# Performance work log

Measured on AMD Instinct MI355X. Metric: run time of the kernel, lower is better.

## Reference

```python
import jax, jax.numpy as jnp
import numpy as np

EPS = 1e-5

def layer_norm(x, gamma, beta):
    mu = jnp.mean(x, axis=-1, keepdims=True)
    var = jnp.mean(jnp.square(x - mu), axis=-1, keepdims=True)
    return (x - mu) * jax.lax.rsqrt(var + EPS) * gamma + beta

def setup_inputs() -> dict:
    key = jax.random.key(0)
    ks = jax.random.split(key, 16)
    B, Cq, Hq, Wq = 8, 256, 32, 32
    Cc, Hc, Wc = 512, 64, 64
    def lin(k, fan_in, fan_out):
        lim = 1.0 / np.sqrt(fan_in)
        k1, k2 = jax.random.split(k)
        W = jax.random.uniform(k1, (fan_in, fan_out), jnp.float32, -lim, lim)
        b = jax.random.uniform(k2, (fan_out,), jnp.float32, -lim, lim)
        return W, b
    Wq_, bq = lin(ks[0], Cq, Cq)
    Wk_, bk = lin(ks[1], Cc, Cq)
    Wv_, bv = lin(ks[2], Cc, Cq)
    Wo_, bo = lin(ks[3], Cq, Cq)
    return {
        "query": jax.random.normal(ks[4], (B, Cq, Hq, Wq), jnp.float32),
        "context": jax.random.normal(ks[5], (B, Cc, Hc, Wc), jnp.float32),
        "Wq": Wq_, "bq": bq, "Wk": Wk_, "bk": bk, "Wv": Wv_, "bv": bv,
        "Wo": Wo_, "bo": bo,
        "gq": jnp.ones((Cq,), jnp.float32), "betq": jnp.zeros((Cq,), jnp.float32),
        "gc": jnp.ones((Cc,), jnp.float32), "betc": jnp.zeros((Cc,), jnp.float32),
    }

def reference(query, context, Wq, bq, Wk, bk, Wv, bv, Wo, bo, gq, betq, gc, betc):
    B, Cq, Hq, Wq_sp = query.shape
    _, Cc, Hc, Wc = context.shape
    num_heads = 8
    head_dim = Cq // num_heads
    scale = jnp.sqrt(jnp.float32(head_dim))
    N = Hq * Wq_sp
    # adaptive_avg_pool2d with divisible sizes == average pooling over equal bins
    ctx = context.reshape(B, Cc, Hq, Hc // Hq, Wq_sp, Wc // Wq_sp).mean(axis=(3, 5))
    q_flat = query.reshape(B, Cq, N).transpose(0, 2, 1)          # (B,N,Cq)
    c_flat = ctx.reshape(B, Cc, N).transpose(0, 2, 1)            # (B,N,Cc)
    qn = layer_norm(q_flat, gq, betq)
    cn = layer_norm(c_flat, gc, betc)
    q = (qn @ Wq + bq).reshape(B, N, num_heads, head_dim).transpose(0, 2, 1, 3)
    k = (cn @ Wk + bk).reshape(B, N, num_heads, head_dim).transpose(0, 2, 1, 3)
    v = (cn @ Wv + bv).reshape(B, N, num_heads, head_dim).transpose(0, 2, 1, 3)
    attn = jnp.einsum('bhnd,bhmd->bhnm', q, k) / scale
    attn = jax.nn.softmax(attn, axis=-1)
    out = jnp.einsum('bhnm,bhmd->bhnd', attn, v)
    out = out.transpose(0, 2, 1, 3).reshape(B, N, Cq)
    out = out @ Wo + bo
    out = q_flat + out                                           # residual
    return out.transpose(0, 2, 1).reshape(B, Cq, Hq, Wq_sp)
```

## Files before the change

### kernel.cpp

```cpp
#include <hip/hip_runtime.h>
#include <hip/hip_bf16.h>
#include <cstddef>

#define B_  8
#define CQ  256
#define CC  512
#define N_  1024
#define HQ  32
#define WQ  32
#define NH  8
#define HD  32

typedef __bf16 bf16x8 __attribute__((ext_vector_type(8)));
typedef float f32x4 __attribute__((ext_vector_type(4)));
typedef float f32x16 __attribute__((ext_vector_type(16)));
typedef unsigned int uint4v __attribute__((ext_vector_type(4)));
typedef unsigned short ushort8 __attribute__((ext_vector_type(8)));
typedef unsigned short ushort4v __attribute__((ext_vector_type(4)));
typedef unsigned short ushort2v __attribute__((ext_vector_type(2)));

__device__ __forceinline__ unsigned short f2bf(float x) {
    return __builtin_bit_cast(unsigned short, __float2bfloat16(x));
}
__device__ __forceinline__ float bf2f(unsigned short x) {
    return __bfloat162float(__builtin_bit_cast(__hip_bfloat16, x));
}
__device__ __forceinline__ bf16x8 ldb8(const unsigned short* p) {
    return __builtin_bit_cast(bf16x8, *(const ushort8*)p);
}

__global__ __launch_bounds__(256) void prep_k(
    const float* __restrict__ query, const float* __restrict__ context,
    const float* __restrict__ Wq, const float* __restrict__ Wk,
    const float* __restrict__ Wv, const float* __restrict__ Wo,
    const float* __restrict__ gq, const float* __restrict__ betq,
    const float* __restrict__ gc, const float* __restrict__ betc,
    __hip_bfloat16* __restrict__ Wqt, __hip_bfloat16* __restrict__ Wkt,
    __hip_bfloat16* __restrict__ Wvt, __hip_bfloat16* __restrict__ Wot,
    __hip_bfloat16* __restrict__ qn, __hip_bfloat16* __restrict__ cn) {
    __shared__ __align__(16) char sm[36352];
    const int bid = blockIdx.x;
    const int tid = threadIdx.x;

    if (bid < 512) {
        float (*T)[33] = (float (*)[33])sm;
        const int x = bid & 15, y = (bid >> 4) & 7, z = bid >> 7;
        const float* W; __hip_bfloat16* Wt; int K;
        switch (z) {
            case 0: W = Wq; Wt = Wqt; K = CQ; break;
            case 1: W = Wk; Wt = Wkt; K = CC; break;
            case 2: W = Wv; Wt = Wvt; K = CC; break;
            default: W = Wo; Wt = Wot; K = CQ; break;
        }
        const int k0 = x * 32;
        if (k0 >= K) return;
        const int c0 = y * 32;
        const int tx = tid & 31, ty = tid >> 5;
        #pragma unroll
        for (int i = 0; i < 4; ++i) {
            const int r = ty + 8 * i;
            T[r][tx] = W[(size_t)(k0 + r) * CQ + c0 + tx];
        }
        __syncthreads();
        #pragma unroll
        for (int i = 0; i < 4; ++i) {
            const int r = ty + 8 * i;
            Wt[(size_t)(c0 + r) * K + k0 + tx] = __float2bfloat16(T[tx][r]);
        }
    } else if (bid < 768) {
        const int u = bid - 512;
        const int hq = u & 31, b = u >> 5;
        unsigned short (*P)[32] = (unsigned short (*)[32])sm;
        float (*Ss)[32]  = (float (*)[32])(sm + 32768);
        float (*S2s)[32] = (float (*)[32])(sm + 33792);
        float* Mu = (float*)(sm + 34816);
        float* Rs = (float*)(sm + 34944);
        const int wq = tid & 31, cty = tid >> 5;

        const float* Cb = context + (size_t)b * CC * 64 * 64;
        float s = 0.f, s2 = 0.f;
        #pragma unroll 4
        for (int it = 0; it < 64; ++it) {
            const int cc = it * 8 + cty;
            const float* r0 = Cb + ((size_t)cc * 64 + 2 * hq) * 64 + 2 * wq;
            const float2 a  = *(const float2*)(r0);
            const float2 bv = *(const float2*)(r0 + 64);
            const float v = (a.x + a.y + bv.x + bv.y) * 0.25f;
            P[cc][wq ^ (cc & 31)] = f2bf(v);
            s += v; s2 += v * v;
        }
        Ss[cty][wq] = s; S2s[cty][wq] = s2;
        __syncthreads();
        if (cty == 0) {
            float ts = 0.f, t2 = 0.f;
            #pragma unroll
            for (int i = 0; i < 8; ++i) { ts += Ss[i][wq]; t2 += S2s[i][wq]; }
            const float mu  = ts * (1.f / CC);
            const float var = t2 * (1.f / CC) - mu * mu;
            Mu[wq] = mu; Rs[wq] = rsqrtf(var + 1e-5f);
        }
        __syncthreads();
        unsigned short* outb = (unsigned short*)cn + ((size_t)b * N_ + hq * 32) * CC;
        #pragma unroll 4
        for (int it = 0; it < 32; ++it) {
            const int idx = it * 256 + tid;
            const int row = idx >> 8;
            const int c   = (idx & 255) * 2;
            const float v0 = bf2f(P[c][row ^ (c & 31)]);
            const float v1 = bf2f(P[c + 1][row ^ ((c + 1) & 31)]);
            const float mu = Mu[row], rs = Rs[row];
            ushort2v o;
            o.x = f2bf((v0 - mu) * rs * gc[c] + betc[c]);
            o.y = f2bf((v1 - mu) * rs * gc[c + 1] + betc[c + 1]);
            *(ushort2v*)(outb + (size_t)row * CC + c) = o;
        }
    } else {
        const int u = bid - 768;
        const int n0 = (u & 15) * 64, b = u >> 4;
        unsigned short (*Qt)[264] = (unsigned short (*)[264])sm;
        float (*Ss)[64]  = (float (*)[64])(sm + 33792);
        float (*S2s)[64] = (float (*)[64])(sm + 34816);
        float* Mu = (float*)(sm + 35840);
        float* Rs = (float*)(sm + 36096);
        const int tx = tid & 63, ty = tid >> 6;

        const float* Qb = query + (size_t)b * CQ * N_;
        float s = 0.f, s2 = 0.f;
        for (int c = ty; c < CQ; c += 4) {
            const float v = Qb[(size_t)c * N_ + n0 + tx];
            Qt[tx][c] = f2bf(v);
            s += v; s2 += v * v;
        }
        Ss[ty][tx] = s; S2s[ty][tx] = s2;
        __syncthreads();
        if (ty == 0) {
            float ts = 0.f, t2 = 0.f;
            #pragma unroll
            for (int i = 0; i < 4; ++i) { ts += Ss[i][tx]; t2 += S2s[i][tx]; }
            const float mu  = ts * (1.f / CQ);
            const float var = t2 * (1.f / CQ) - mu * mu;
            Mu[tx] = mu; Rs[tx] = rsqrtf(var + 1e-5f);
        }
        __syncthreads();
        unsigned short* outb = (unsigned short*)qn + ((size_t)b * N_ + n0) * CQ;
        #pragma unroll
        for (int it = 0; it < 8; ++it) {
            const int idx = it * 256 + tid;
            const int row = idx >> 5;
            const int c0  = (idx & 31) * 8;
            const ushort8 v = *(const ushort8*)&Qt[row][c0];
            const float mu = Mu[row], rs = Rs[row];
            ushort8 o;
            #pragma unroll
            for (int e = 0; e < 8; ++e)
                o[e] = f2bf((bf2f(v[e]) - mu) * rs * gq[c0 + e] + betq[c0 + e]);
            *(ushort8*)(outb + (size_t)row * CQ + c0) = o;
        }
    }
}

__global__ __launch_bounds__(256) void proj_all_k(
    const __hip_bfloat16* __restrict__ qn, const __hip_bfloat16* __restrict__ cn,
    const __hip_bfloat16* __restrict__ Wqt, const __hip_bfloat16* __restrict__ Wkt,
    const __hip_bfloat16* __restrict__ Wvt,
    const float* __restrict__ bq, const float* __restrict__ bk,
    const float* __restrict__ bv,
    __hip_bfloat16* __restrict__ Qb, __hip_bfloat16* __restrict__ Kb,
    __hip_bfloat16* __restrict__ Vt, float qsc) {
    __shared__ unsigned short As[64][40];
    __shared__ unsigned short B1[64][40];
    __shared__ unsigned short B2[64][40];

    const int zz = blockIdx.z;
    const int n0 = blockIdx.x * 64;
    const int c0 = blockIdx.y * 64;
    const int tid = threadIdx.x;
    const int wid = tid >> 6, lane = tid & 63;
    const int lg = lane >> 4, ln = lane & 15;
    const int wn0 = (wid & 1) * 32, wc0 = (wid >> 1) * 32;
    const int sr = tid >> 2;
    const int sk = (tid & 3) * 8;

    if (zz >= 8) {
        const int b = zz - 8;
        const unsigned short* Ab = (const unsigned short*)qn + ((size_t)b * N_ + n0) * CQ;
        const unsigned short* Wb = (const unsigned short*)Wqt + (size_t)c0 * CQ;
        f32x4 acc[2][2] = {};
        ushort8 ra = *(const ushort8*)(Ab + (size_t)sr * CQ + sk);
        ushort8 rw = *(const ushort8*)(Wb + (size_t)sr * CQ + sk);
        for (int t = 0; t < 8; ++t) {
            *(ushort8*)&As[sr][sk] = ra;
            *(ushort8*)&B1[sr][sk] = rw;
            __syncthreads();
            if (t < 7) {
                ra = *(const ushort8*)(Ab + (size_t)sr * CQ + (t + 1) * 32 + sk);
                rw = *(const ushort8*)(Wb + (size_t)sr * CQ + (t + 1) * 32 + sk);
            }
            bf16x8 a[2], w[2];
            #pragma unroll
            for (int i = 0; i < 2; ++i) a[i] = ldb8(&As[wn0 + 16 * i + ln][8 * lg]);
            #pragma unroll
            for (int j = 0; j < 2; ++j) w[j] = ldb8(&B1[wc0 + 16 * j + ln][8 * lg]);
            #pragma unroll
            for (int i = 0; i < 2; ++i)
                #pragma unroll
                for (int j = 0; j < 2; ++j)
                    acc[i][j] = __builtin_amdgcn_mfma_f32_16x16x32_bf16(a[i], w[j], acc[i][j], 0, 0, 0);
            __syncthreads();
        }
        #pragma unroll
        for (int j = 0; j < 2; ++j) {
            const int co = c0 + wc0 + 16 * j + ln;
            const int h = co >> 5, d = co & 31;
            const float bb = bq[co];
            #pragma unroll
            for (int i = 0; i < 2; ++i)
                #pragma unroll
                for (int r = 0; r < 4; ++r) {
                    const int n = n0 + wn0 + 16 * i + 4 * lg + r;
                    Qb[(((size_t)b * NH + h) * N_ + n) * HD + d] =
                        __float2bfloat16((acc[i][j][r] + bb) * qsc);
                }
        }
    } else {
        const int b = zz;
        const unsigned short* Ab  = (const unsigned short*)cn + ((size_t)b * N_ + n0) * CC;
        const unsigned short* Wkb = (const unsigned short*)Wkt + (size_t)c0 * CC;
        const unsigned short* Wvb = (const unsigned short*)Wvt + (size_t)c0 * CC;
        f32x4 accK[2][2] = {};
        f32x4 accV[2][2] = {};
        ushort8 ra = *(const ushort8*)(Ab  + (size_t)sr * CC + sk);
        ushort8 rk = *(const ushort8*)(Wkb + (size_t)sr * CC + sk);
        ushort8 rv = *(const ushort8*)(Wvb + (size_t)sr * CC + sk);
        for (int t = 0; t < 16; ++t) {
            *(ushort8*)&As[sr][sk] = ra;
            *(ushort8*)&B1[sr][sk] = rk;
            *(ushort8*)&B2[sr][sk] = rv;
            __syncthreads();
            if (t < 15) {
                ra = *(const ushort8*)(Ab  + (size_t)sr * CC + (t + 1) * 32 + sk);
                rk = *(const ushort8*)(Wkb + (size_t)sr * CC + (t + 1) * 32 + sk);
                rv = *(const ushort8*)(Wvb + (size_t)sr * CC + (t + 1) * 32 + sk);
            }
            bf16x8 a[2], wk[2], wv[2];
            #pragma unroll
            for (int i = 0; i < 2; ++i) {
                a[i]  = ldb8(&As[wn0 + 16 * i + ln][8 * lg]);
                wk[i] = ldb8(&B1[wc0 + 16 * i + ln][8 * lg]);
                wv[i] = ldb8(&B2[wc0 + 16 * i + ln][8 * lg]);
            }
            #pragma unroll
            for (int i = 0; i < 2; ++i)
                #pragma unroll
                for (int j = 0; j < 2; ++j) {
                    accK[i][j] = __builtin_amdgcn_mfma_f32_16x16x32_bf16(a[i], wk[j], accK[i][j], 0, 0, 0);
                    accV[i][j] = __builtin_amdgcn_mfma_f32_16x16x32_bf16(a[i], wv[j], accV[i][j], 0, 0, 0);
                }
            __syncthreads();
        }
        #pragma unroll
        for (int j = 0; j < 2; ++j) {
            const int co = c0 + wc0 + 16 * j + ln;
            const int h = co >> 5, d = co & 31;
            const float bbk = bk[co], bbv = bv[co];
            #pragma unroll
            for (int i = 0; i < 2; ++i) {
                const int nb = n0 + wn0 + 16 * i + 4 * lg;
                #pragma unroll
                for (int r = 0; r < 4; ++r)
                    Kb[(((size_t)b * NH + h) * N_ + nb + r) * HD + d] =
                        __float2bfloat16(accK[i][j][r] + bbk);
                ushort4v o;
                #pragma unroll
                for (int r = 0; r < 4; ++r) o[r] = f2bf(accV[i][j][r] + bbv);
                const int g  = (nb >> 2) & 3;
                const int gp = ((g & 1) << 1) | (g >> 1);
                const int nbp = (nb & ~15) | (gp << 2);
                *(ushort4v*)((unsigned short*)Vt + (((size_t)b * NH + h) * HD + d) * N_ + nbp) = o;
            }
        }
    }
}

__global__ __launch_bounds__(256) void attn32_k(
    const __hip_bfloat16* __restrict__ Q,
    const __hip_bfloat16* __restrict__ K,
    const __hip_bfloat16* __restrict__ Vt,
    __hip_bfloat16* __restrict__ O) {
    __shared__ float accS[2][64][20];
    __shared__ float lwS[2][64];

    const int lin = blockIdx.x + 16 * blockIdx.y;
    const int eff = (lin & 7) * 128 + (lin >> 3);
    const int qt  = eff & 15;
    const int bh  = eff >> 4;
    const int b   = bh >> 3;
    const int h   = bh & 7;
    const int wid  = threadIdx.x >> 6;
    const int lane = threadIdx.x & 63;
    const int l31  = lane & 31;
    const int hh   = lane >> 5;
    const int qsub = wid >> 1;
    const int kvh  = wid & 1;
    const int q0   = qt * 64 + qsub * 32;

    const unsigned short* Qp = (const unsigned short*)Q + ((size_t)bh * N_ + q0) * HD;
    const unsigned short* Kbb = (const unsigned short*)K + (size_t)bh * N_ * HD;
    const unsigned short* Vb = (const unsigned short*)Vt + ((size_t)bh * HD + l31) * N_;

    bf16x8 qB[2];
    #pragma unroll
    for (int m = 0; m < 2; ++m)
        qB[m] = ldb8(Qp + (size_t)l31 * HD + 16 * m + 8 * hh);

    const f32x16 Z = {0.f,0.f,0.f,0.f,0.f,0.f,0.f,0.f,
                      0.f,0.f,0.f,0.f,0.f,0.f,0.f,0.f};
    f32x16 acc = Z;
    float ls0 = 0.f, ls1 = 0.f, ls2 = 0.f, ls3 = 0.f;

    const int kvbase = kvh * 512;
    const unsigned short* kp = Kbb + (size_t)(kvbase + l31) * HD + 8 * hh;
    const unsigned short* vp = Vb + kvbase + 8 * hh;

    bf16x8 kaA[2][4];
    #pragma unroll
    for (int j = 0; j < 4; ++j)
        kaA[0][j] = ldb8(kp + (j >> 1) * 1024 + (j & 1) * 16);

    #pragma unroll
    for (int st = 0; st < 8; ++st) {
        const int cur = st & 1;
        bf16x8 va[4];
        #pragma unroll
        for (int j = 0; j < 4; ++j)
            va[j] = ldb8(vp + st * 64 + 16 * j);
        if (st < 7) {
            const unsigned short* kp2 = kp + (size_t)(st + 1) * 2048;
            #pragma unroll
            for (int j = 0; j < 4; ++j)
                kaA[cur ^ 1][j] = ldb8(kp2 + (j >> 1) * 1024 + (j & 1) * 16);
        }

        f32x16 s0, s1;
        s0 = __builtin_amdgcn_mfma_f32_32x32x16_bf16(kaA[cur][0], qB[0], Z, 0, 0, 0);
        s0 = __builtin_amdgcn_mfma_f32_32x32x16_bf16(kaA[cur][1], qB[1], s0, 0, 0, 0);
        s1 = __builtin_amdgcn_mfma_f32_32x32x16_bf16(kaA[cur][2], qB[0], Z, 0, 0, 0);
        s1 = __builtin_amdgcn_mfma_f32_32x32x16_bf16(kaA[cur][3], qB[1], s1, 0, 0, 0);

        unsigned int pk[2][4][2];
        #pragma unroll
        for (int T = 0; T < 2; ++T) {
            float p[16];
            #pragma unroll
            for (int r = 0; r < 16; ++r)
                p[r] = __builtin_amdgcn_exp2f(T == 0 ? s0[r] : s1[r]);
            #pragma unroll
            for (int r = 0; r < 16; r += 4) {
                ls0 += p[r]; ls1 += p[r + 1]; ls2 += p[r + 2]; ls3 += p[r + 3];
            }
            #pragma unroll
            for (int c = 0; c < 4; ++c) {
                asm("v_cvt_pk_bf16_f32 %0, %1, %2"
                    : "=v"(pk[T][c][0]) : "v"(p[4 * c]), "v"(p[4 * c + 1]));
                asm("v_cvt_pk_bf16_f32 %0, %1, %2"
                    : "=v"(pk[T][c][1]) : "v"(p[4 * c + 2]), "v"(p[4 * c + 3]));
            }
        }

        #pragma unroll
        for (int w = 0; w < 4; ++w) {
            const int T = w >> 1, cp = w & 1;
            uint4v fu = {pk[T][2 * cp][0], pk[T][2 * cp][1],
                         pk[T][2 * cp + 1][0], pk[T][2 * cp + 1][1]};
            const bf16x8 pa = __builtin_bit_cast(bf16x8, fu);
            acc = __builtin_amdgcn_mfma_f32_32x32x16_bf16(pa, va[w], acc, 0, 0, 0);
        }
    }

    const float lsum = (ls0 + ls1) + (ls2 + ls3);
    const float lw = lsum + __shfl_xor(lsum, 32);

    if (kvh == 1) {
        #pragma unroll
        for (int r4 = 0; r4 < 4; ++r4) {
            float4 v = {acc[4 * r4], acc[4 * r4 + 1], acc[4 * r4 + 2], acc[4 * r4 + 3]};
            *(float4*)&accS[qsub][lane][4 * r4] = v;
        }
        lwS[qsub][lane] = lw;
    }
    __syncthreads();
    if (kvh == 0) {
        const float linv = 1.0f / (lw + lwS[qsub][lane]);
        #pragma unroll
        for (int r = 0; r < 16; ++r) {
            const int ql = (r & 3) + 8 * (r >> 2) + 4 * hh;
            const float vv = (acc[r] + accS[qsub][lane][r]) * __shfl(linv, ql);
            O[((size_t)b * N_ + q0 + ql) * CQ + h * HD + l31] = __float2bfloat16(vv);
        }
    }
}

__global__ __launch_bounds__(256) void out_proj_k(const __hip_bfloat16* __restrict__ Ob,
                              const __hip_bfloat16* __restrict__ Wot,
                              const float* __restrict__ bo,
                              const float* __restrict__ query,
                              float* __restrict__ out) {
    __shared__ unsigned short As[64][40];
    __shared__ unsigned short Bs[64][40];
    const int b  = blockIdx.z;
    const int n0 = blockIdx.x * 64;
    const int c0 = blockIdx.y * 64;
    const int tid = threadIdx.x;
    const int wid = tid >> 6, lane = tid & 63;
    const int lg = lane >> 4, ln = lane & 15;
    const int wn0 = (wid & 1) * 32, wc0 = (wid >> 1) * 32;

    const unsigned short* Ab = (const unsigned short*)Ob + ((size_t)b * N_ + n0) * CQ;
    const unsigned short* Wb = (const unsigned short*)Wot + (size_t)c0 * CQ;
    const int sr = tid >> 2;
    const int sk = (tid & 3) * 8;

    f32x4 acc[2][2] = {};
    ushort8 ra = *(const ushort8*)(Ab + (size_t)sr * CQ + sk);
    ushort8 rw = *(const ushort8*)(Wb + (size_t)sr * CQ + sk);

    for (int t = 0; t < 8; ++t) {
        *(ushort8*)&As[sr][sk] = ra;
        *(ushort8*)&Bs[sr][sk] = rw;
        __syncthreads();
        if (t < 7) {
            ra = *(const ushort8*)(Ab + (size_t)sr * CQ + (t + 1) * 32 + sk);
            rw = *(const ushort8*)(Wb + (size_t)sr * CQ + (t + 1) * 32 + sk);
        }
        bf16x8 a[2], w[2];
        #pragma unroll
        for (int i = 0; i < 2; ++i)
            a[i] = ldb8(&As[wn0 + 16 * i + ln][8 * lg]);
        #pragma unroll
        for (int j = 0; j < 2; ++j)
            w[j] = ldb8(&Bs[wc0 + 16 * j + ln][8 * lg]);
        #pragma unroll
        for (int i = 0; i < 2; ++i)
            #pragma unroll
            for (int j = 0; j < 2; ++j)
                acc[i][j] = __builtin_amdgcn_mfma_f32_16x16x32_bf16(a[i], w[j], acc[i][j], 0, 0, 0);
        __syncthreads();
    }

    #pragma unroll
    for (int j = 0; j < 2; ++j) {
        const int co = c0 + wc0 + 16 * j + ln;
        const float bb = bo[co];
        #pragma unroll
        for (int i = 0; i < 2; ++i) {
            const int nb = n0 + wn0 + 16 * i + 4 * lg;
            const float4 res = *(const float4*)&query[((size_t)b * CQ + co) * N_ + nb];
            float4 o;
            o.x = acc[i][j][0] + bb + res.x;
            o.y = acc[i][j][1] + bb + res.y;
            o.z = acc[i][j][2] + bb + res.z;
            o.w = acc[i][j][3] + bb + res.w;
            *(float4*)&out[((size_t)b * CQ + co) * N_ + nb] = o;
        }
    }
}

extern "C" void kernel_launch(void* const* d_in, const int* in_sizes, int n_in,
                              void* d_out, int out_size, void* d_ws, size_t ws_size,
                              hipStream_t stream) {
    const float* query   = (const float*)d_in[0];
    const float* context = (const float*)d_in[1];
    const float* Wq = (const float*)d_in[2];
    const float* bq = (const float*)d_in[3];
    const float* Wk = (const float*)d_in[4];
    const float* bk = (const float*)d_in[5];
    const float* Wv = (const float*)d_in[6];
    const float* bv = (const float*)d_in[7];
    const float* Wo = (const float*)d_in[8];
    const float* bo = (const float*)d_in[9];
    const float* gq   = (const float*)d_in[10];
    const float* betq = (const float*)d_in[11];
    const float* gc   = (const float*)d_in[12];
    const float* betc = (const float*)d_in[13];
    float* out = (float*)d_out;

    char* w = (char*)d_ws;
    __hip_bfloat16* qn  = (__hip_bfloat16*)w;  w += (size_t)B_ * N_ * CQ * 2;
    __hip_bfloat16* cn  = (__hip_bfloat16*)w;  w += (size_t)B_ * N_ * CC * 2;
    __hip_bfloat16* Qb  = (__hip_bfloat16*)w;  w += (size_t)B_ * NH * N_ * HD * 2;
    __hip_bfloat16* Kb  = (__hip_bfloat16*)w;  w += (size_t)B_ * NH * N_ * HD * 2;
    __hip_bfloat16* Vt  = (__hip_bfloat16*)w;  w += (size_t)B_ * NH * HD * N_ * 2;
    __hip_bfloat16* Ob  = (__hip_bfloat16*)w;  w += (size_t)B_ * N_ * CQ * 2;
    __hip_bfloat16* Wqt = (__hip_bfloat16*)w;  w += (size_t)CQ * CQ * 2;
    __hip_bfloat16* Wkt = (__hip_bfloat16*)w;  w += (size_t)CQ * CC * 2;
    __hip_bfloat16* Wvt = (__hip_bfloat16*)w;  w += (size_t)CQ * CC * 2;
    __hip_bfloat16* Wot = (__hip_bfloat16*)w;  w += (size_t)CQ * CQ * 2;

    prep_k<<<dim3(896), 256, 0, stream>>>(query, context, Wq, Wk, Wv, Wo,
                                          gq, betq, gc, betc,
                                          Wqt, Wkt, Wvt, Wot, qn, cn);

    const float qsc = 0.17677669529663687f * 1.4426950408889634f;
    proj_all_k<<<dim3(16, 4, 16), 256, 0, stream>>>(qn, cn, Wqt, Wkt, Wvt,
                                                    bq, bk, bv, Qb, Kb, Vt, qsc);

    attn32_k<<<dim3(16, 64), 256, 0, stream>>>(Qb, Kb, Vt, Ob);

    out_proj_k<<<dim3(16, 4, 8), 256, 0, stream>>>(Ob, Wot, bo, query, out);
}
```

Measured before the change: 78.03 us.

## Restructure LayerNorm prep to register-held tiles with smaller shared memory

The context-pool and query LayerNorm paths in the prep kernel now keep each thread's 16 channel values in registers instead of staging a transposed bf16 tile in shared memory. Each block covers a smaller tile (8 pixels of context or 16 query positions), so the grid grows from 896 to 2048 blocks and shared memory drops from about 36 KB to a few KB. This aims to raise occupancy and parallelism and to drop a shared-memory round trip, while letting each thread write 16 contiguous bf16 outputs. The trade-off is less coalesced global reads, since context reads now use 8 pixels per channel row, plus more blocks that each do redundant gamma/beta loads.

```diff
diff --git a/kernel.cpp b/kernel.cpp
--- a/kernel.cpp
+++ b/kernel.cpp
@@ -38,12 +38,15 @@
     __hip_bfloat16* __restrict__ Wqt, __hip_bfloat16* __restrict__ Wkt,
     __hip_bfloat16* __restrict__ Wvt, __hip_bfloat16* __restrict__ Wot,
     __hip_bfloat16* __restrict__ qn, __hip_bfloat16* __restrict__ cn) {
-    __shared__ __align__(16) char sm[36352];
+    __shared__ float T[32][33];
+    __shared__ float Ss[32][16];
+    __shared__ float S2s[32][16];
+    __shared__ float Mu[16], Rs[16];
+
     const int bid = blockIdx.x;
     const int tid = threadIdx.x;
 
     if (bid < 512) {
-        float (*T)[33] = (float (*)[33])sm;
         const int x = bid & 15, y = (bid >> 4) & 7, z = bid >> 7;
         const float* W; __hip_bfloat16* Wt; int K;
         switch (z) {
@@ -67,95 +70,90 @@
             const int r = ty + 8 * i;
             Wt[(size_t)(c0 + r) * K + k0 + tx] = __float2bfloat16(T[tx][r]);
         }
-    } else if (bid < 768) {
-        const int u = bid - 512;
-        const int hq = u & 31, b = u >> 5;
-        unsigned short (*P)[32] = (unsigned short (*)[32])sm;
-        float (*Ss)[32]  = (float (*)[32])(sm + 32768);
-        float (*S2s)[32] = (float (*)[32])(sm + 33792);
-        float* Mu = (float*)(sm + 34816);
-        float* Rs = (float*)(sm + 34944);
-        const int wq = tid & 31, cty = tid >> 5;
-
-        const float* Cb = context + (size_t)b * CC * 64 * 64;
+    } else if (bid < 1536) {
+        const int u   = bid - 512;
+        const int wqc = u & 3, hq = (u >> 2) & 31, b = u >> 7;
+        const int p   = tid & 7;
+        const int cg  = tid >> 3;
+        const int wq  = wqc * 8 + p;
+        const int c0  = cg * 16;
+
+        const float* Cb = context + ((size_t)b * CC + c0) * 4096
+                        + (size_t)(2 * hq) * 64 + 2 * wq;
+        float pv[16];
         float s = 0.f, s2 = 0.f;
-        #pragma unroll 4
-        for (int it = 0; it < 64; ++it) {
-            const int cc = it * 8 + cty;
-            const float* r0 = Cb + ((size_t)cc * 64 + 2 * hq) * 64 + 2 * wq;
+        #pragma unroll
+        for (int i = 0; i < 16; ++i) {
+            const float* r0 = Cb + (size_t)i * 4096;
             const float2 a  = *(const float2*)(r0);
             const float2 bv = *(const float2*)(r0 + 64);
             const float v = (a.x + a.y + bv.x + bv.y) * 0.25f;
-            P[cc][wq ^ (cc & 31)] = f2bf(v);
+            pv[i] = v;
             s += v; s2 += v * v;
         }
-        Ss[cty][wq] = s; S2s[cty][wq] = s2;
-        __syncthreads();
-        if (cty == 0) {
+        Ss[cg][p] = s; S2s[cg][p] = s2;
+        __syncthreads();
+        if (tid < 8) {
             float ts = 0.f, t2 = 0.f;
             #pragma unroll
-            for (int i = 0; i < 8; ++i) { ts += Ss[i][wq]; t2 += S2s[i][wq]; }
+            for (int i = 0; i < 32; ++i) { ts += Ss[i][tid]; t2 += S2s[i][tid]; }
             const float mu  = ts * (1.f / CC);
             const float var = t2 * (1.f / CC) - mu * mu;
-            Mu[wq] = mu; Rs[wq] = rsqrtf(var + 1e-5f);
-        }
-        __syncthreads();
-        unsigned short* outb = (unsigned short*)cn + ((size_t)b * N_ + hq * 32) * CC;
-        #pragma unroll 4
-        for (int it = 0; it < 32; ++it) {
-            const int idx = it * 256 + tid;
-            const int row = idx >> 8;
-            const int c   = (idx & 255) * 2;
-            const float v0 = bf2f(P[c][row ^ (c & 31)]);
-            const float v1 = bf2f(P[c + 1][row ^ ((c + 1) & 31)]);
-            const float mu = Mu[row], rs = Rs[row];
-            ushort2v o;
-            o.x = f2bf((v0 - mu) * rs * gc[c] + betc[c]);
-            o.y = f2bf((v1 - mu) * rs * gc[c + 1] + betc[c + 1]);
-            *(ushort2v*)(outb + (size_t)row * CC + c) = o;
-        }
+            Mu[tid] = mu; Rs[tid] = rsqrtf(var + 1e-5f);
+        }
+        __syncthreads();
+        const float mu = Mu[p], rs = Rs[p];
+        ushort8 o0, o1;
+        #pragma unroll
+        for (int i = 0; i < 8; ++i)
+            o0[i] = f2bf((pv[i] - mu) * rs * gc[c0 + i] + betc[c0 + i]);
+        #pragma unroll
+        for (int i = 0; i < 8; ++i)
+            o1[i] = f2bf((pv[8 + i] - mu) * rs * gc[c0 + 8 + i] + betc[c0 + 8 + i]);
+        unsigned short* dst = (unsigned short*)cn
+            + ((size_t)b * N_ + hq * 32 + wq) * CC + c0;
+        *(ushort8*)(dst)     = o0;
+        *(ushort8*)(dst + 8) = o1;
     } else {
-        const int u = bid - 768;
-        const int n0 = (u & 15) * 64, b = u >> 4;
-        unsigned short (*Qt)[264] = (unsigned short (*)[264])sm;
-        float (*Ss)[64]  = (float (*)[64])(sm + 33792);
-        float (*S2s)[64] = (float (*)[64])(sm + 34816);
-        float* Mu = (float*)(sm + 35840);
-        float* Rs = (float*)(sm + 36096);
-        const int tx = tid & 63, ty = tid >> 6;
-
-        const float* Qb = query + (size_t)b * CQ * N_;
+        const int u  = bid - 1536;
+        const int nt = u & 63, b = u >> 6;
+        const int n0 = nt * 16;
+        const int nn = tid & 15;
+        const int cg = tid >> 4;
+        const int c0 = cg * 16;
+
+        const float* Qb = query + ((size_t)b * CQ + c0) * N_ + n0 + nn;
+        float qv[16];
         float s = 0.f, s2 = 0.f;
-        for (int c = ty; c < CQ; c += 4) {
-            const float v = Qb[(size_t)c * N_ + n0 + tx];
-            Qt[tx][c] = f2bf(v);
+        #pragma unroll
+        for (int i = 0; i < 16; ++i) {
+            const float v = Qb[(size_t)i * N_];
+            qv[i] = v;
             s += v; s2 += v * v;
         }
-        Ss[ty][tx] = s; S2s[ty][tx] = s2;
-        __syncthreads();
-        if (ty == 0) {
+        Ss[cg][nn] = s; S2s[cg][nn] = s2;
+        __syncthreads();
+        if (tid < 16) {
             float ts = 0.f, t2 = 0.f;
             #pragma unroll
-            for (int i = 0; i < 4; ++i) { ts += Ss[i][tx]; t2 += S2s[i][tx]; }
+            for (int i = 0; i < 16; ++i) { ts += Ss[i][tid]; t2 += S2s[i][tid]; }
             const float mu  = ts * (1.f / CQ);
             const float var = t2 * (1.f / CQ) - mu * mu;
-            Mu[tx] = mu; Rs[tx] = rsqrtf(var + 1e-5f);
-        }
-        __syncthreads();
-        unsigned short* outb = (unsigned short*)qn + ((size_t)b * N_ + n0) * CQ;
-        #pragma unroll
-        for (int it = 0; it < 8; ++it) {
-            const int idx = it * 256 + tid;
-            const int row = idx >> 5;
-            const int c0  = (idx & 31) * 8;
-            const ushort8 v = *(const ushort8*)&Qt[row][c0];
-            const float mu = Mu[row], rs = Rs[row];
-            ushort8 o;
-            #pragma unroll
-            for (int e = 0; e < 8; ++e)
-                o[e] = f2bf((bf2f(v[e]) - mu) * rs * gq[c0 + e] + betq[c0 + e]);
-            *(ushort8*)(outb + (size_t)row * CQ + c0) = o;
-        }
+            Mu[tid] = mu; Rs[tid] = rsqrtf(var + 1e-5f);
+        }
+        __syncthreads();
+        const float mu = Mu[nn], rs = Rs[nn];
+        ushort8 o0, o1;
+        #pragma unroll
+        for (int i = 0; i < 8; ++i)
+            o0[i] = f2bf((qv[i] - mu) * rs * gq[c0 + i] + betq[c0 + i]);
+        #pragma unroll
+        for (int i = 0; i < 8; ++i)
+            o1[i] = f2bf((qv[8 + i] - mu) * rs * gq[c0 + 8 + i] + betq[c0 + 8 + i]);
+        unsigned short* dst = (unsigned short*)qn
+            + ((size_t)b * N_ + n0 + nn) * CQ + c0;
+        *(ushort8*)(dst)     = o0;
+        *(ushort8*)(dst + 8) = o1;
     }
 }
 
@@ -496,9 +494,9 @@
     __hip_bfloat16* Wvt = (__hip_bfloat16*)w;  w += (size_t)CQ * CC * 2;
     __hip_bfloat16* Wot = (__hip_bfloat16*)w;  w += (size_t)CQ * CQ * 2;
 
-    prep_k<<<dim3(896), 256, 0, stream>>>(query, context, Wq, Wk, Wv, Wo,
-                                          gq, betq, gc, betc,
-                                          Wqt, Wkt, Wvt, Wot, qn, cn);
+    prep_k<<<dim3(2048), 256, 0, stream>>>(query, context, Wq, Wk, Wv, Wo,
+                                           gq, betq, gc, betc,
+                                           Wqt, Wkt, Wvt, Wot, qn, cn);
 
     const float qsc = 0.17677669529663687f * 1.4426950408889634f;
     proj_all_k<<<dim3(16, 4, 16), 256, 0, stream>>>(qn, cn, Wqt, Wkt, Wvt,
```

New measurement: 76.83 us. About the same (-1.5%).
